# Kernel tuning notes

Hardware: AMD Instinct MI355X
Metric: run time of the kernel (lower is better)

Reference implementation:

```python
import jax, jax.numpy as jnp
import numpy as np
from jax import lax

B, C, H, W, S = 8, 64, 64, 64, 12
KSIZE = 5


def _conv2d_same(x, w):
    # x: [N, Cin, H, W], w: [Cout, Cin, kh, kw]
    return lax.conv_general_dilated(
        x, w, window_strides=(1, 1), padding='SAME',
        dimension_numbers=('NCHW', 'OIHW', 'NCHW'))


def setup_inputs() -> dict:
    key = jax.random.key(0)
    k0, k1, k2, k3, k4 = jax.random.split(key, 5)
    x = jax.random.normal(k0, (B, C, H, W, S), dtype=jnp.float32)
    w1 = jax.random.normal(k1, (3 * C, C, 1, 1), dtype=jnp.float32) * 0.05
    b1 = jax.random.normal(k2, (3 * C,), dtype=jnp.float32) * 0.05
    w2 = jax.random.normal(k3, (1, 2 * C, KSIZE, KSIZE), dtype=jnp.float32) * 0.05
    b2 = jax.random.normal(k4, (1,), dtype=jnp.float32) * 0.05
    return {'x': x, 'w1': w1, 'b1': b1, 'w2': w2, 'b2': b2}


def reference(x, w1, b1, w2, b2):
    b, c, h, w_, s = x.shape
    # conv1 (1x1) applied per timestep == channel matmul over all timesteps at once
    qkv = jnp.einsum('oc,bchws->bohws', w1[:, :, 0, 0], x) + b1[None, :, None, None, None]
    Q, K, V = jnp.split(qkv, 3, axis=1)  # each [b, c, h, w, s]

    # conv2 on concat(Q_s, K_t) is linear in channels:
    # score(s,t) = convQ(Q[...,s]) + convK(K[...,t]) + bias
    def per_time_conv(z, wsub):
        # z: [b, c, h, w, s] -> fold time into batch -> conv -> [b, h, w, s]
        zb = jnp.moveaxis(z, -1, 1).reshape(b * s, c, h, w_)
        out = _conv2d_same(zb, wsub)  # [b*s, 1, h, w]
        return jnp.moveaxis(out.reshape(b, s, h, w_), 1, -1)  # [b, h, w, s]

    A_q = per_time_conv(Q, w2[:, :c])   # [b, h, w, s] (query index)
    A_k = per_time_conv(K, w2[:, c:])   # [b, h, w, t] (key index)

    # scores: [b, h, w, t, s]
    scores = A_q[:, :, :, None, :] + A_k[:, :, :, :, None] + b2[0]
    attn = jax.nn.softmax(scores, axis=-2)  # softmax over t (keys)

    # weighted sum of V over t -> [b, c, h, w, s]
    V_out = jnp.einsum('bhwts,bchwt->bchws', attn, V)
    return V_out
```

## Files before the change

### kernel.cpp

```cpp
#include <hip/hip_runtime.h>
#include <hip/hip_bf16.h>

#define U_OFF    4096
#define U_PLANE  393216
#define WS_WEFF_OFF 393216
#define WEFF_FALLBACK_OFF 0

__global__ __launch_bounds__(256) void k_prep(const float* __restrict__ w1,
                                              const float* __restrict__ w2,
                                              float* __restrict__ wdst) {
    int idx = blockIdx.x * 256 + threadIdx.x;
    if (idx >= 64 * 25) return;
    int cp = idx / 25, tap = idx % 25;
    float s = 0.f;
    for (int c = 0; c < 64; ++c)
        s = fmaf(w2[(64 + c) * 25 + tap], w1[(64 + c) * 64 + cp], s);
    wdst[cp * 25 + tap] = s;
}

__global__ __launch_bounds__(256) void k_tap(const float* __restrict__ x,
                                             const float* __restrict__ weff,
                                             float* __restrict__ u) {
    const int gid = blockIdx.x * 256 + threadIdx.x;
    const int m   = gid / 12;
    const int t   = gid - m * 12;
    const int w   = m & 63;
    const int h   = (m >> 6) & 63;
    const int b   = m >> 12;

    const float* xp = x + (size_t)b * 3145728 + h * 768 + w * 12 + t;

    const bool ok0 = (w >= 2), ok1 = (w >= 1), ok3 = (w <= 62), ok4 = (w <= 61);
    const int  o0 = ok0 ? -24 : 0, o1 = ok1 ? -12 : 0;
    const int  o3 = ok3 ?  12 : 0, o4 = ok4 ?  24 : 0;

    float u0 = 0.f, u1 = 0.f, u2 = 0.f, u3 = 0.f, u4 = 0.f;

    for (int cb = 0; cb < 16; ++cb) {
        float xv[4][5];
#pragma unroll
        for (int j = 0; j < 4; ++j) {
            const float* base = xp + (size_t)(cb * 4 + j) * 49152;
            float v0 = base[o0], v1 = base[o1], v2 = base[0];
            float v3 = base[o3], v4 = base[o4];
            xv[j][0] = ok0 ? v0 : 0.f;
            xv[j][1] = ok1 ? v1 : 0.f;
            xv[j][2] = v2;
            xv[j][3] = ok3 ? v3 : 0.f;
            xv[j][4] = ok4 ? v4 : 0.f;
        }
#pragma unroll
        for (int j = 0; j < 4; ++j) {
            const float* wg = weff + (cb * 4 + j) * 25;
#pragma unroll
            for (int dw = 0; dw < 5; ++dw) {
                const float v = xv[j][dw];
                u0 = fmaf(wg[0 * 5 + dw], v, u0);
                u1 = fmaf(wg[1 * 5 + dw], v, u1);
                u2 = fmaf(wg[2 * 5 + dw], v, u2);
                u3 = fmaf(wg[3 * 5 + dw], v, u3);
                u4 = fmaf(wg[4 * 5 + dw], v, u4);
            }
        }
    }

    u[(size_t)0 * U_PLANE + gid] = u0;
    u[(size_t)1 * U_PLANE + gid] = u1;
    u[(size_t)2 * U_PLANE + gid] = u2;
    u[(size_t)3 * U_PLANE + gid] = u3;
    u[(size_t)4 * U_PLANE + gid] = u4;
}

__global__ __launch_bounds__(256) void k_gather(const float* __restrict__ u,
                                                float* __restrict__ p) {
    const int tid  = threadIdx.x;
    const int m    = blockIdx.x * 64 + (tid >> 2);
    const int q    = tid & 3;
    const int qq   = (q == 3) ? 2 : q;
    const int w    = m & 63;
    const int h    = (m >> 6) & 63;
    const int b    = m >> 12;

    float4 a; a.x = 0.f; a.y = 0.f; a.z = 0.f; a.w = 0.f;

#pragma unroll
    for (int dh = 0; dh < 5; ++dh) {
        const int hh = h + dh - 2;
        if ((unsigned)hh >= 64u) continue;
        const float* up = u + (size_t)dh * U_PLANE
                            + (size_t)(((b * 64 + hh) * 64 + w)) * 12 + qq * 4;
        float4 v = *(const float4*)(up);
        a.x += v.x; a.y += v.y; a.z += v.z; a.w += v.w;
    }

    float mx = fmaxf(fmaxf(a.x, a.y), fmaxf(a.z, a.w));
    mx = fmaxf(mx, __shfl_xor(mx, 1, 4));
    mx = fmaxf(mx, __shfl_xor(mx, 2, 4));

    float e0 = __expf(a.x - mx), e1 = __expf(a.y - mx);
    float e2 = __expf(a.z - mx), e3 = __expf(a.w - mx);
    const float s4 = e0 + e1 + e2 + e3;
    const float s0 = __shfl(s4, 0, 4);
    const float s1 = __shfl(s4, 1, 4);
    const float s2 = __shfl(s4, 2, 4);
    const float inv = 1.f / (s0 + s1 + s2);

    if (q < 3) {
        float4 o; o.x = e0 * inv; o.y = e1 * inv; o.z = e2 * inv; o.w = e3 * inv;
        *(float4*)(p + (size_t)m * 12 + q * 4) = o;
    }
}

__global__ __launch_bounds__(512) void k_out(const float* __restrict__ x,
                                             const float* __restrict__ w1,
                                             const float* __restrict__ b1,
                                             const float* __restrict__ p,
                                             float* __restrict__ out) {
    __shared__ float lds[64 * 65];

    const int b  = blockIdx.x >> 6;
    const int h  = blockIdx.x & 63;
    const int w  = threadIdx.x & 63;
    const int cg = threadIdx.x >> 6;

    const float* pp = p + (size_t)((b * 64 + h) * 64 + w) * 12;
    float pv[12];
    {
        float4 t0 = *(const float4*)(pp);
        float4 t1 = *(const float4*)(pp + 4);
        float4 t2 = *(const float4*)(pp + 8);
        pv[0] = t0.x; pv[1] = t0.y; pv[2]  = t0.z; pv[3]  = t0.w;
        pv[4] = t1.x; pv[5] = t1.y; pv[6]  = t1.z; pv[7]  = t1.w;
        pv[8] = t2.x; pv[9] = t2.y; pv[10] = t2.z; pv[11] = t2.w;
    }

    const float* xb0 = x + ((size_t)(b * 64 + cg * 8) * 64 + h) * 768 + w * 12;
#pragma unroll
    for (int j = 0; j < 8; ++j) {
        const float* xp = xb0 + (size_t)j * 49152;
        float4 u0 = *(const float4*)(xp);
        float4 u1 = *(const float4*)(xp + 4);
        float4 u2 = *(const float4*)(xp + 8);
        float s = 0.f;
        s = fmaf(pv[0], u0.x, s);  s = fmaf(pv[1], u0.y, s);
        s = fmaf(pv[2], u0.z, s);  s = fmaf(pv[3], u0.w, s);
        s = fmaf(pv[4], u1.x, s);  s = fmaf(pv[5], u1.y, s);
        s = fmaf(pv[6], u1.z, s);  s = fmaf(pv[7], u1.w, s);
        s = fmaf(pv[8], u2.x, s);  s = fmaf(pv[9], u2.y, s);
        s = fmaf(pv[10], u2.z, s); s = fmaf(pv[11], u2.w, s);
        lds[w * 65 + cg * 8 + j] = s;
    }
    __syncthreads();

    const float* w1v = w1 + 128 * 64 + cg * 8 * 64;
    float acc[8];
#pragma unroll
    for (int j = 0; j < 8; ++j) acc[j] = b1[128 + cg * 8 + j];
    for (int c2 = 0; c2 < 64; ++c2) {
        const float xv = lds[w * 65 + c2];
#pragma unroll
        for (int j = 0; j < 8; ++j)
            acc[j] = fmaf(w1v[j * 64 + c2], xv, acc[j]);
    }

#pragma unroll
    for (int j = 0; j < 8; ++j) {
        const int co = cg * 8 + j;
        float4 f; f.x = acc[j]; f.y = acc[j]; f.z = acc[j]; f.w = acc[j];
        float* op = out + ((size_t)(b * 64 + co) * 4096 + h * 64 + w) * 12;
        *(float4*)(op)     = f;
        *(float4*)(op + 4) = f;
        *(float4*)(op + 8) = f;
    }
}

extern "C" void kernel_launch(void* const* d_in, const int* in_sizes, int n_in,
                              void* d_out, int out_size, void* d_ws, size_t ws_size,
                              hipStream_t stream) {
    const float* x  = (const float*)d_in[0];
    const float* w1 = (const float*)d_in[1];
    const float* b1 = (const float*)d_in[2];
    const float* w2 = (const float*)d_in[3];

    float* outp = (float*)d_out;
    float* u    = outp + U_OFF;
    float* p    = (float*)d_ws;

    const bool ws_fits = ws_size >= (size_t)(WS_WEFF_OFF + 1600) * sizeof(float);
    float* weff = ws_fits ? (p + WS_WEFF_OFF) : (outp + WEFF_FALLBACK_OFF);

    hipLaunchKernelGGL(k_prep,   dim3(7),    dim3(256), 0, stream, w1, w2, weff);
    hipLaunchKernelGGL(k_tap,    dim3(1536), dim3(256), 0, stream, x, weff, u);
    hipLaunchKernelGGL(k_gather, dim3(512),  dim3(256), 0, stream, u, p);
    hipLaunchKernelGGL(k_out,    dim3(512),  dim3(512), 0, stream, x, w1, b1, p, outp);
}
```

Baseline: 97.31 us.

## Split k_tap channel reduction into two halves with partial planes summed in gather

The k_tap grid is doubled so that each half of the blocks reduces over 32 of the 64 input channels. Each half writes its own set of five partial tap planes into the scratch area, and k_gather now loads and adds both partial planes before the softmax. This shortens the serial per-thread channel loop and gives the GPU more blocks in flight to hide memory latency. In exchange it doubles the partial-sum write traffic and the gather read traffic, and it uses more of the output buffer as scratch.

```diff
diff --git a/kernel.cpp b/kernel.cpp
--- a/kernel.cpp
+++ b/kernel.cpp
@@ -21,14 +21,16 @@
 __global__ __launch_bounds__(256) void k_tap(const float* __restrict__ x,
                                              const float* __restrict__ weff,
                                              float* __restrict__ u) {
-    const int gid = blockIdx.x * 256 + threadIdx.x;
+    const int chalf = (blockIdx.x >= 1536) ? 1 : 0;
+    const int gid   = (blockIdx.x - chalf * 1536) * 256 + threadIdx.x;
     const int m   = gid / 12;
     const int t   = gid - m * 12;
     const int w   = m & 63;
     const int h   = (m >> 6) & 63;
     const int b   = m >> 12;
 
-    const float* xp = x + (size_t)b * 3145728 + h * 768 + w * 12 + t;
+    const float* xp = x + (size_t)b * 3145728 + h * 768 + w * 12 + t
+                        + (size_t)(chalf * 32) * 49152;
 
     const bool ok0 = (w >= 2), ok1 = (w >= 1), ok3 = (w <= 62), ok4 = (w <= 61);
     const int  o0 = ok0 ? -24 : 0, o1 = ok1 ? -12 : 0;
@@ -36,7 +38,8 @@
 
     float u0 = 0.f, u1 = 0.f, u2 = 0.f, u3 = 0.f, u4 = 0.f;
 
-    for (int cb = 0; cb < 16; ++cb) {
+    const float* wbase = weff + chalf * 32 * 25;
+    for (int cb = 0; cb < 8; ++cb) {
         float xv[4][5];
 #pragma unroll
         for (int j = 0; j < 4; ++j) {
@@ -51,7 +54,7 @@
         }
 #pragma unroll
         for (int j = 0; j < 4; ++j) {
-            const float* wg = weff + (cb * 4 + j) * 25;
+            const float* wg = wbase + (cb * 4 + j) * 25;
 #pragma unroll
             for (int dw = 0; dw < 5; ++dw) {
                 const float v = xv[j][dw];
@@ -64,11 +67,12 @@
         }
     }
 
-    u[(size_t)0 * U_PLANE + gid] = u0;
-    u[(size_t)1 * U_PLANE + gid] = u1;
-    u[(size_t)2 * U_PLANE + gid] = u2;
-    u[(size_t)3 * U_PLANE + gid] = u3;
-    u[(size_t)4 * U_PLANE + gid] = u4;
+    float* ub = u + (size_t)(chalf * 5) * U_PLANE + gid;
+    ub[(size_t)0 * U_PLANE] = u0;
+    ub[(size_t)1 * U_PLANE] = u1;
+    ub[(size_t)2 * U_PLANE] = u2;
+    ub[(size_t)3 * U_PLANE] = u3;
+    ub[(size_t)4 * U_PLANE] = u4;
 }
 
 __global__ __launch_bounds__(256) void k_gather(const float* __restrict__ u,
@@ -87,10 +91,13 @@
     for (int dh = 0; dh < 5; ++dh) {
         const int hh = h + dh - 2;
         if ((unsigned)hh >= 64u) continue;
-        const float* up = u + (size_t)dh * U_PLANE
-                            + (size_t)(((b * 64 + hh) * 64 + w)) * 12 + qq * 4;
-        float4 v = *(const float4*)(up);
-        a.x += v.x; a.y += v.y; a.z += v.z; a.w += v.w;
+        const size_t moff = (size_t)(((b * 64 + hh) * 64 + w)) * 12 + qq * 4;
+        const float* up0 = u + (size_t)dh * U_PLANE + moff;
+        const float* up1 = u + (size_t)(5 + dh) * U_PLANE + moff;
+        float4 v0 = *(const float4*)(up0);
+        float4 v1 = *(const float4*)(up1);
+        a.x += v0.x + v1.x; a.y += v0.y + v1.y;
+        a.z += v0.z + v1.z; a.w += v0.w + v1.w;
     }
 
     float mx = fmaxf(fmaxf(a.x, a.y), fmaxf(a.z, a.w));
@@ -190,7 +197,7 @@
     float* weff = ws_fits ? (p + WS_WEFF_OFF) : (outp + WEFF_FALLBACK_OFF);
 
     hipLaunchKernelGGL(k_prep,   dim3(7),    dim3(256), 0, stream, w1, w2, weff);
-    hipLaunchKernelGGL(k_tap,    dim3(1536), dim3(256), 0, stream, x, weff, u);
+    hipLaunchKernelGGL(k_tap,    dim3(3072), dim3(256), 0, stream, x, weff, u);
     hipLaunchKernelGGL(k_gather, dim3(512),  dim3(256), 0, stream, u, p);
     hipLaunchKernelGGL(k_out,    dim3(512),  dim3(512), 0, stream, x, w1, b1, p, outp);
 }
```

New measurement: 97.73 us. Within noise of the previous version (+0.4%).

## Vectorize tap kernel over timesteps and split channels into four partial sums

Applied to the files above, without the earlier changes.

Each k_tap thread now computes four consecutive timesteps with float4 loads and FMAs, and covers only a quarter of the 64 input channels. It writes 20 partial planes instead of 5, and k_gather sums the four channel-quarter partials for each vertical tap. The aim is fewer load instructions, more instruction-level parallelism and a shorter per-thread reduction chain. The cost is about four times more intermediate u traffic: four times the writes in k_tap and four times the reads in k_gather.

```diff
diff --git a/kernel.cpp b/kernel.cpp
--- a/kernel.cpp
+++ b/kernel.cpp
@@ -21,54 +21,67 @@
 __global__ __launch_bounds__(256) void k_tap(const float* __restrict__ x,
                                              const float* __restrict__ weff,
                                              float* __restrict__ u) {
-    const int gid = blockIdx.x * 256 + threadIdx.x;
-    const int m   = gid / 12;
-    const int t   = gid - m * 12;
-    const int w   = m & 63;
-    const int h   = (m >> 6) & 63;
-    const int b   = m >> 12;
-
-    const float* xp = x + (size_t)b * 3145728 + h * 768 + w * 12 + t;
+    const int n     = blockIdx.x * 256 + threadIdx.x;
+    const int cq    = n / 98304;
+    const int inner = n - cq * 98304;
+    const int b     = inner / 12288;
+    const int ln    = inner - b * 12288;
+    const int w     = (ln / 3) & 63;
+
+    const float* xp = x + (size_t)b * 3145728 + (size_t)(cq * 16) * 49152
+                        + (size_t)ln * 4;
 
     const bool ok0 = (w >= 2), ok1 = (w >= 1), ok3 = (w <= 62), ok4 = (w <= 61);
     const int  o0 = ok0 ? -24 : 0, o1 = ok1 ? -12 : 0;
     const int  o3 = ok3 ?  12 : 0, o4 = ok4 ?  24 : 0;
 
-    float u0 = 0.f, u1 = 0.f, u2 = 0.f, u3 = 0.f, u4 = 0.f;
-
-    for (int cb = 0; cb < 16; ++cb) {
-        float xv[4][5];
-#pragma unroll
-        for (int j = 0; j < 4; ++j) {
-            const float* base = xp + (size_t)(cb * 4 + j) * 49152;
-            float v0 = base[o0], v1 = base[o1], v2 = base[0];
-            float v3 = base[o3], v4 = base[o4];
-            xv[j][0] = ok0 ? v0 : 0.f;
-            xv[j][1] = ok1 ? v1 : 0.f;
-            xv[j][2] = v2;
-            xv[j][3] = ok3 ? v3 : 0.f;
-            xv[j][4] = ok4 ? v4 : 0.f;
+    float4 u0, u1, u2, u3, u4;
+    u0.x=0.f;u0.y=0.f;u0.z=0.f;u0.w=0.f; u1=u0; u2=u0; u3=u0; u4=u0;
+
+    const float* wbase = weff + cq * 16 * 25;
+    const float4 zero = u0;
+
+    for (int j = 0; j < 16; ++j) {
+        const float* base = xp + (size_t)j * 49152;
+        float4 x0 = *(const float4*)(base + o0);
+        float4 x1 = *(const float4*)(base + o1);
+        float4 x2 = *(const float4*)(base);
+        float4 x3 = *(const float4*)(base + o3);
+        float4 x4 = *(const float4*)(base + o4);
+        if (!ok0) x0 = zero;
+        if (!ok1) x1 = zero;
+        if (!ok3) x3 = zero;
+        if (!ok4) x4 = zero;
+
+        const float* wg = wbase + j * 25;
+#pragma unroll
+        for (int dh = 0; dh < 5; ++dh) {
+            const float g0 = wg[dh * 5 + 0];
+            const float g1 = wg[dh * 5 + 1];
+            const float g2 = wg[dh * 5 + 2];
+            const float g3 = wg[dh * 5 + 3];
+            const float g4 = wg[dh * 5 + 4];
+            float4* uacc = (dh == 0) ? &u0 : (dh == 1) ? &u1 : (dh == 2) ? &u2
+                          : (dh == 3) ? &u3 : &u4;
+            uacc->x = fmaf(g0, x0.x, uacc->x); uacc->y = fmaf(g0, x0.y, uacc->y);
+            uacc->z = fmaf(g0, x0.z, uacc->z); uacc->w = fmaf(g0, x0.w, uacc->w);
+            uacc->x = fmaf(g1, x1.x, uacc->x); uacc->y = fmaf(g1, x1.y, uacc->y);
+            uacc->z = fmaf(g1, x1.z, uacc->z); uacc->w = fmaf(g1, x1.w, uacc->w);
+            uacc->x = fmaf(g2, x2.x, uacc->x); uacc->y = fmaf(g2, x2.y, uacc->y);
+            uacc->z = fmaf(g2, x2.z, uacc->z); uacc->w = fmaf(g2, x2.w, uacc->w);
+            uacc->x = fmaf(g3, x3.x, uacc->x); uacc->y = fmaf(g3, x3.y, uacc->y);
+            uacc->z = fmaf(g3, x3.z, uacc->z); uacc->w = fmaf(g3, x3.w, uacc->w);
+            uacc->x = fmaf(g4, x4.x, uacc->x); uacc->y = fmaf(g4, x4.y, uacc->y);
+            uacc->z = fmaf(g4, x4.z, uacc->z); uacc->w = fmaf(g4, x4.w, uacc->w);
         }
-#pragma unroll
-        for (int j = 0; j < 4; ++j) {
-            const float* wg = weff + (cb * 4 + j) * 25;
-#pragma unroll
-            for (int dw = 0; dw < 5; ++dw) {
-                const float v = xv[j][dw];
-                u0 = fmaf(wg[0 * 5 + dw], v, u0);
-                u1 = fmaf(wg[1 * 5 + dw], v, u1);
-                u2 = fmaf(wg[2 * 5 + dw], v, u2);
-                u3 = fmaf(wg[3 * 5 + dw], v, u3);
-                u4 = fmaf(wg[4 * 5 + dw], v, u4);
-            }
-        }
-    }
-
-    u[(size_t)0 * U_PLANE + gid] = u0;
-    u[(size_t)1 * U_PLANE + gid] = u1;
-    u[(size_t)2 * U_PLANE + gid] = u2;
-    u[(size_t)3 * U_PLANE + gid] = u3;
-    u[(size_t)4 * U_PLANE + gid] = u4;
+    }
+
+    float* ub = u + (size_t)(cq * 5) * U_PLANE + (size_t)inner * 4;
+    *(float4*)(ub + (size_t)0 * U_PLANE) = u0;
+    *(float4*)(ub + (size_t)1 * U_PLANE) = u1;
+    *(float4*)(ub + (size_t)2 * U_PLANE) = u2;
+    *(float4*)(ub + (size_t)3 * U_PLANE) = u3;
+    *(float4*)(ub + (size_t)4 * U_PLANE) = u4;
 }
 
 __global__ __launch_bounds__(256) void k_gather(const float* __restrict__ u,
@@ -87,10 +100,12 @@
     for (int dh = 0; dh < 5; ++dh) {
         const int hh = h + dh - 2;
         if ((unsigned)hh >= 64u) continue;
-        const float* up = u + (size_t)dh * U_PLANE
-                            + (size_t)(((b * 64 + hh) * 64 + w)) * 12 + qq * 4;
-        float4 v = *(const float4*)(up);
-        a.x += v.x; a.y += v.y; a.z += v.z; a.w += v.w;
+        const size_t moff = (size_t)(((b * 64 + hh) * 64 + w)) * 12 + qq * 4;
+#pragma unroll
+        for (int cq = 0; cq < 4; ++cq) {
+            float4 v = *(const float4*)(u + (size_t)(cq * 5 + dh) * U_PLANE + moff);
+            a.x += v.x; a.y += v.y; a.z += v.z; a.w += v.w;
+        }
     }
 
     float mx = fmaxf(fmaxf(a.x, a.y), fmaxf(a.z, a.w));
```

After: 106.4 us. +9.3%, slower.
